# Performance work log

Hardware: AMD Instinct MI355X
Metric: run time of the kernel (lower is better)

## Reference

```python
import jax, jax.numpy as jnp
import numpy as np

EMBED_DIM = 1024
NUM_TOKENS = 32
TOKEN_DIM = 32  # ceil(1024/32)
CODEBOOK_SIZE = 256
BATCH = 32768
BETA = 0.25


def setup_inputs() -> dict:
    key = jax.random.key(0)
    ks = jax.random.split(key, 6)
    lim_e = 1.0 / np.sqrt(EMBED_DIM)
    lim_d = 1.0 / np.sqrt(NUM_TOKENS * TOKEN_DIM)
    lim_c = 1.0 / CODEBOOK_SIZE
    return {
        "skills": jax.random.normal(ks[0], (BATCH, EMBED_DIM), jnp.float32),
        "enc_w": jax.random.uniform(ks[1], (NUM_TOKENS * TOKEN_DIM, EMBED_DIM), jnp.float32, -lim_e, lim_e),
        "enc_b": jax.random.uniform(ks[2], (NUM_TOKENS * TOKEN_DIM,), jnp.float32, -lim_e, lim_e),
        "codebook": jax.random.uniform(ks[3], (CODEBOOK_SIZE, TOKEN_DIM), jnp.float32, -lim_c, lim_c),
        "dec_w": jax.random.uniform(ks[4], (EMBED_DIM, NUM_TOKENS * TOKEN_DIM), jnp.float32, -lim_d, lim_d),
        "dec_b": jax.random.uniform(ks[5], (EMBED_DIM,), jnp.float32, -lim_d, lim_d),
    }


def reference(skills, enc_w, enc_b, codebook, dec_w, dec_b):
    B = skills.shape[0]
    # encoder linear -> [B, num_tokens, token_dim]
    projected = (skills @ enc_w.T + enc_b).reshape(B, NUM_TOKENS, TOKEN_DIM)
    flat = projected.reshape(-1, TOKEN_DIM)  # [B*T, d]
    # squared-euclidean distances to codebook entries: [B*T, K]
    dists = (
        jnp.sum(flat * flat, axis=1, keepdims=True)
        - 2.0 * flat @ codebook.T
        + jnp.sum(codebook * codebook, axis=1)[None, :]
    )
    codes = jnp.argmin(dists, axis=1)  # [B*T]
    quantized = codebook[codes].reshape(B, NUM_TOKENS, TOKEN_DIM)
    # straight-through estimator
    st = projected + jax.lax.stop_gradient(quantized - projected)
    commitment = jnp.mean((projected - jax.lax.stop_gradient(quantized)) ** 2)
    codebook_loss = jnp.mean((quantized - jax.lax.stop_gradient(projected)) ** 2)
    vq_loss = codebook_loss + BETA * commitment
    reconstructed = st.reshape(B, NUM_TOKENS * TOKEN_DIM) @ dec_w.T + dec_b
    recon_loss = jnp.mean((reconstructed - skills) ** 2)
    loss = vq_loss + recon_loss
    return reconstructed, codes.reshape(B, NUM_TOKENS), loss
```

## Files before the change

### kernel.cpp

```cpp
#include <hip/hip_runtime.h>
#include <hip/hip_bf16.h>
#include <float.h>

#define NROWS 32768
#define EMB 1024
#define CBN 256
#define TD 32

#define OUT_CODES_OFF (33554432UL)
#define OUT_LOSS_OFF  (34603008UL)
#define TAU 1e-5f
#define INV_N (1.0f/33554432.0f)

typedef __attribute__((ext_vector_type(8))) short s16x8;
typedef __attribute__((ext_vector_type(4))) float f32x4;

__device__ __forceinline__ unsigned short bf16r(float x) {
    unsigned int u = __float_as_uint(x);
    unsigned int r = (u + 0x7FFFu + ((u >> 16) & 1u)) >> 16;
    return (unsigned short)r;
}
__device__ __forceinline__ float bf16f(unsigned short h) {
    return __uint_as_float(((unsigned int)h) << 16);
}
__device__ __forceinline__ void split8r(float4 v0, float4 v1, s16x8& h, s16x8& l) {
    float xs[8] = {v0.x, v0.y, v0.z, v0.w, v1.x, v1.y, v1.z, v1.w};
    #pragma unroll
    for (int e = 0; e < 8; ++e) {
        unsigned int u = __float_as_uint(xs[e]);
        unsigned short hh = (unsigned short)(u >> 16);
        h[e] = (short)hh;
        l[e] = (short)bf16r(xs[e] - bf16f(hh));
    }
}

__launch_bounds__(512, 1)
__global__ void k_enc(const float* __restrict__ skills,
                      const float* __restrict__ enc_w,
                      const float* __restrict__ enc_b,
                      const float* __restrict__ cb_g,
                      float* __restrict__ out)
{
    __shared__ __align__(16) char smem[125952];
    typedef unsigned short (*pu40)[40];
    pu40 Ah = (pu40)(smem);
    pu40 Al = (pu40)(smem + 10240);
    pu40 Bh = (pu40)(smem + 20480);
    pu40 Bl = (pu40)(smem + 30720);
    pu40 Sh = (pu40)(smem);
    pu40 Sl = (pu40)(smem + 40960);
    pu40 Ch = (pu40)(smem + 81920);
    pu40 Cl = (pu40)(smem + 102400);
    float* cnb = (float*)(smem + 122880);
    float* Fv  = (float*)(smem + 123904);

    const int tid = threadIdx.x;
    const int r0 = blockIdx.x * 128;
    const int wid = tid >> 6, lane = tid & 63;
    const int wm = wid >> 1, wn = wid & 1;
    const int mbase = wm * 32, nbase = wn * 64;
    const int lhi = lane >> 4, llo = lane & 15;
    const int srow = tid >> 2, sq = tid & 3;

    if (tid < 256) {
        const float4* cr = (const float4*)&cb_g[tid * 32];
        float s = 0.f;
        #pragma unroll
        for (int i = 0; i < 8; ++i) {
            float4 v = cr[i];
            float c[4] = {v.x, v.y, v.z, v.w};
            #pragma unroll
            for (int e = 0; e < 4; ++e) {
                unsigned int u = __float_as_uint(c[e]);
                unsigned short hh = (unsigned short)(u >> 16);
                Ch[tid][i*4+e] = hh;
                Cl[tid][i*4+e] = bf16r(c[e] - bf16f(hh));
                s = fmaf(c[e], c[e], s);
            }
        }
        cnb[tid] = s;
    }
    __syncthreads();

    float vq_local = 0.f;
    f32x4 acc[2][4];
    float4 ra0, ra1, rb0, rb1;

    {
        const float* ap = &skills[(size_t)(r0 + srow) * 1024 + sq * 8];
        ra0 = *(const float4*)ap; ra1 = *(const float4*)(ap + 4);
        const float* bp = &enc_w[(size_t)srow * 1024 + sq * 8];
        rb0 = *(const float4*)bp; rb1 = *(const float4*)(bp + 4);
    }

    for (int it = 0; it < 256; ++it) {
        const int nt = it >> 5, kt = it & 31;
        const int n0 = nt * 128;
        if (kt == 0) {
            #pragma unroll
            for (int mf = 0; mf < 2; ++mf)
                #pragma unroll
                for (int nf = 0; nf < 4; ++nf) acc[mf][nf] = (f32x4)0.f;
        }
        __syncthreads();
        {
            s16x8 h, l;
            split8r(ra0, ra1, h, l);
            *(s16x8*)&Ah[srow][sq * 8] = h;
            *(s16x8*)&Al[srow][sq * 8] = l;
            split8r(rb0, rb1, h, l);
            *(s16x8*)&Bh[srow][sq * 8] = h;
            *(s16x8*)&Bl[srow][sq * 8] = l;
        }
        __syncthreads();
        if (it < 255) {
            const int it2 = it + 1, nt2 = it2 >> 5, kt2 = it2 & 31;
            const float* ap = &skills[(size_t)(r0 + srow) * 1024 + kt2 * 32 + sq * 8];
            ra0 = *(const float4*)ap; ra1 = *(const float4*)(ap + 4);
            const float* bp = &enc_w[(size_t)(nt2 * 128 + srow) * 1024 + kt2 * 32 + sq * 8];
            rb0 = *(const float4*)bp; rb1 = *(const float4*)(bp + 4);
        }
        {
            s16x8 ah[2], al[2], bh[4], bl[4];
            #pragma unroll
            for (int mf = 0; mf < 2; ++mf) {
                const int row = mbase + mf * 16 + llo;
                ah[mf] = *(s16x8*)&Ah[row][lhi * 8];
                al[mf] = *(s16x8*)&Al[row][lhi * 8];
            }
            #pragma unroll
            for (int nf = 0; nf < 4; ++nf) {
                const int row = nbase + nf * 16 + llo;
                bh[nf] = *(s16x8*)&Bh[row][lhi * 8];
                bl[nf] = *(s16x8*)&Bl[row][lhi * 8];
            }
            #pragma unroll
            for (int mf = 0; mf < 2; ++mf)
                #pragma unroll
                for (int nf = 0; nf < 4; ++nf) {
                    acc[mf][nf] = __builtin_amdgcn_mfma_f32_16x16x32_bf16(ah[mf], bh[nf], acc[mf][nf], 0, 0, 0);
                    acc[mf][nf] = __builtin_amdgcn_mfma_f32_16x16x32_bf16(ah[mf], bl[nf], acc[mf][nf], 0, 0, 0);
                    acc[mf][nf] = __builtin_amdgcn_mfma_f32_16x16x32_bf16(al[mf], bh[nf], acc[mf][nf], 0, 0, 0);
                }
        }

        if (kt == 31) {
            __syncthreads();
            float fp[2][4][2];
            #pragma unroll
            for (int mf = 0; mf < 2; ++mf)
                #pragma unroll
                for (int r = 0; r < 4; ++r) { fp[mf][r][0] = 0.f; fp[mf][r][1] = 0.f; }

            #pragma unroll
            for (int mf = 0; mf < 2; ++mf)
                #pragma unroll
                for (int nf = 0; nf < 4; ++nf) {
                    const int n_local = nbase + nf * 16 + llo;
                    const float bias = enc_b[n0 + n_local];
                    const int tl = wn * 2 + (nf >> 1);
                    const int d = ((nf & 1) << 4) + llo;
                    #pragma unroll
                    for (int r = 0; r < 4; ++r) {
                        const int m_local = mbase + mf * 16 + lhi * 4 + r;
                        float val = acc[mf][nf][r] + bias;
                        unsigned int u = __float_as_uint(val);
                        unsigned short hh = (unsigned short)(u >> 16);
                        Sh[m_local * 4 + tl][d] = hh;
                        Sl[m_local * 4 + tl][d] = bf16r(val - bf16f(hh));
                        fp[mf][r][nf >> 1] = fmaf(val, val, fp[mf][r][nf >> 1]);
                    }
                }
            #pragma unroll
            for (int mf = 0; mf < 2; ++mf)
                #pragma unroll
                for (int r = 0; r < 4; ++r)
                    #pragma unroll
                    for (int tt = 0; tt < 2; ++tt) {
                        float f = fp[mf][r][tt];
                        f += __shfl_xor(f, 1); f += __shfl_xor(f, 2);
                        f += __shfl_xor(f, 4); f += __shfl_xor(f, 8);
                        if (llo == 0)
                            Fv[(mbase + mf * 16 + lhi * 4 + r) * 4 + wn * 2 + tt] = f;
                    }
            __syncthreads();

            #pragma unroll
            for (int gi = 0; gi < 4; ++gi) {
                const int g = wid * 4 + gi;
                const int tokrow = g * 16 + llo;
                s16x8 fh = *(s16x8*)&Sh[tokrow][lhi * 8];
                s16x8 fl = *(s16x8*)&Sl[tokrow][lhi * 8];
                float s1[4], s2[4]; int bj[4];
                #pragma unroll
                for (int r = 0; r < 4; ++r) { s1[r] = FLT_MAX; s2[r] = FLT_MAX; bj[r] = 0; }
                for (int jb = 0; jb < 16; ++jb) {
                    const int j = jb * 16 + llo;
                    s16x8 ch = *(s16x8*)&Ch[j][lhi * 8];
                    s16x8 cl = *(s16x8*)&Cl[j][lhi * 8];
                    f32x4 sc = (f32x4)0.f;
                    sc = __builtin_amdgcn_mfma_f32_16x16x32_bf16(fh, ch, sc, 0, 0, 0);
                    sc = __builtin_amdgcn_mfma_f32_16x16x32_bf16(fh, cl, sc, 0, 0, 0);
                    sc = __builtin_amdgcn_mfma_f32_16x16x32_bf16(fl, ch, sc, 0, 0, 0);
                    const float cnv = cnb[j];
                    #pragma unroll
                    for (int r = 0; r < 4; ++r) {
                        float s = fmaf(-2.f, sc[r], cnv);
                        if (s < s1[r])      { s2[r] = s1[r]; s1[r] = s; bj[r] = j; }
                        else if (s < s2[r]) { s2[r] = s; }
                    }
                }
                #pragma unroll
                for (int r = 0; r < 4; ++r) {
                    float a1 = s1[r], a2 = s2[r]; int aj = bj[r];
                    #pragma unroll
                    for (int off = 1; off <= 8; off <<= 1) {
                        float o1 = __shfl_xor(a1, off);
                        float o2 = __shfl_xor(a2, off);
                        int   oj = __shfl_xor(aj, off);
                        if (o1 < a1) { a2 = fminf(a1, o2); a1 = o1; aj = oj; }
                        else         { a2 = fminf(o1, a2); }
                    }
                    if (llo == 0) {
                        const int tok_local = g * 16 + lhi * 4 + r;
                        const float F = Fv[tok_local];
                        float cv = (a2 - a1 < TAU) ? (float)(aj + 512) : (float)aj;
                        const size_t tok = (size_t)(r0 + (tok_local >> 2)) * 32 + nt * 4 + (tok_local & 3);
                        out[OUT_CODES_OFF + tok] = cv;
                        vq_local += F + a1;
                    }
                }
            }
        }
    }
    {
        float v = vq_local;
        #pragma unroll
        for (int off = 32; off >= 1; off >>= 1) v += __shfl_xor(v, off);
        if (lane == 0) atomicAdd(&out[OUT_LOSS_OFF], v * (1.25f * INV_N));
    }
}

__launch_bounds__(256)
__global__ void k_fix(const float* __restrict__ skills,
                      const float* __restrict__ enc_w,
                      const float* __restrict__ enc_b,
                      const float* __restrict__ cb_g,
                      float* __restrict__ codes)
{
    __shared__ unsigned int cnt;
    __shared__ unsigned short list[256];

    const int tid = threadIdx.x;
    const int base = blockIdx.x * 256;

    if (tid == 0) cnt = 0;
    __syncthreads();
    {
        const int c = (int)codes[base + tid];
        if (c >= 512) {
            unsigned int ix = atomicAdd(&cnt, 1u);
            list[ix] = (unsigned short)tid;
        }
    }
    __syncthreads();
    const unsigned int n = cnt;
    if (n == 0) return;

    const int wv = tid >> 6, lane = tid & 63;
    const int d = lane & 31;

    for (unsigned int i = wv; i < n; i += 4) {
        const int tok = base + (int)list[i];
        const int row = tok >> 5;
        const int t   = tok & 31;

        const float4* s4 = (const float4*)&skills[(size_t)row * 1024];
        const float4* w4 = (const float4*)&enc_w[(size_t)(t * 32 + d) * 1024];
        float v1 = 0.f, v2 = 0.f, v3 = 0.f;
        for (int q = 0; q < 96; ++q) {
            float4 a = s4[q], b = w4[q];
            v1 = fmaf(a.x, b.x, v1); v1 = fmaf(a.y, b.y, v1);
            v1 = fmaf(a.z, b.z, v1); v1 = fmaf(a.w, b.w, v1);
        }
        for (int q = 96; q < 192; ++q) {
            float4 a = s4[q], b = w4[q];
            v2 = fmaf(a.x, b.x, v2); v2 = fmaf(a.y, b.y, v2);
            v2 = fmaf(a.z, b.z, v2); v2 = fmaf(a.w, b.w, v2);
        }
        for (int q = 192; q < 256; ++q) {
            float4 a = s4[q], b = w4[q];
            v3 = fmaf(a.x, b.x, v3); v3 = fmaf(a.y, b.y, v3);
            v3 = fmaf(a.z, b.z, v3); v3 = fmaf(a.w, b.w, v3);
        }
        const float pd = ((v1 + v2) + v3) + enc_b[t * 32 + d];

        float pv[32];
        #pragma unroll
        for (int dd = 0; dd < 32; ++dd) pv[dd] = __shfl(pd, dd);

        float F;
        {
            float s[32];
            #pragma unroll
            for (int dd = 0; dd < 32; ++dd) s[dd] = pv[dd] * pv[dd];
            float r[8];
            #pragma unroll
            for (int j = 0; j < 8; ++j) r[j] = ((s[j] + s[8+j]) + s[16+j]) + s[24+j];
            F = ((r[0] + r[1]) + (r[2] + r[3])) + ((r[4] + r[5]) + (r[6] + r[7]));
        }

        float bs = FLT_MAX; int bj = 0;
        for (int m = 0; m < 4; ++m) {
            const int j = m * 64 + lane;
            const float* cj = &cb_g[j * 32];
            float g = 0.f;
            #pragma unroll
            for (int dd = 0; dd < 32; ++dd) g = fmaf(pv[dd], cj[dd], g);
            float cs[32];
            #pragma unroll
            for (int dd = 0; dd < 32; ++dd) cs[dd] = cj[dd] * cj[dd];
            float r[8];
            #pragma unroll
            for (int jj = 0; jj < 8; ++jj) r[jj] = ((cs[jj] + cs[8+jj]) + cs[16+jj]) + cs[24+jj];
            float cn = ((r[0] + r[1]) + (r[2] + r[3])) + ((r[4] + r[5]) + (r[6] + r[7]));
            float dist = (F - 2.0f * g) + cn;
            if (dist < bs) { bs = dist; bj = j; }
        }
        #pragma unroll
        for (int off = 32; off >= 1; off >>= 1) {
            float os = __shfl_xor(bs, off);
            int   oj = __shfl_xor(bj, off);
            if (os < bs || (os == bs && oj < bj)) { bs = os; bj = oj; }
        }
        if (lane == 0) codes[tok] = (float)bj;
    }
}

__launch_bounds__(512)
__global__ void k_dec(const float* __restrict__ skills,
                      const float* __restrict__ cb_g,
                      const float* __restrict__ dec_w,
                      const float* __restrict__ dec_b,
                      const float* __restrict__ codes,
                      float* __restrict__ recon,
                      float* __restrict__ loss_out)
{
    __shared__ unsigned short Qt[128][40], Wt[128][40];

    const int tid = threadIdx.x;
    const int r0 = (blockIdx.x >> 3) * 128;
    const int n0 = (blockIdx.x & 7) * 128;
    const int wid = tid >> 6, lane = tid & 63;
    const int wm = wid >> 1, wn = wid & 1;
    const int mbase = wm * 32, nbase = wn * 64;
    const int lhi = lane >> 4, llo = lane & 15;
    const int srow = tid >> 2, sq = tid & 3;

    f32x4 acc[2][4];
    #pragma unroll
    for (int mf = 0; mf < 2; ++mf)
        #pragma unroll
        for (int nf = 0; nf < 4; ++nf) acc[mf][nf] = (f32x4)0.f;

    float4 q0, q1, w0, w1;
    int cnext;
    {
        const int c0 = ((int)codes[(size_t)(r0 + srow) * 32 + 0]) & 255;
        const float* cp = &cb_g[c0 * 32 + sq * 8];
        q0 = *(const float4*)cp; q1 = *(const float4*)(cp + 4);
        const float* wp = &dec_w[(size_t)(n0 + srow) * 1024 + sq * 8];
        w0 = *(const float4*)wp; w1 = *(const float4*)(wp + 4);
        cnext = ((int)codes[(size_t)(r0 + srow) * 32 + 1]) & 255;
    }

    for (int t = 0; t < 32; ++t) {
        __syncthreads();
        {
            float xs[8] = {q0.x, q0.y, q0.z, q0.w, q1.x, q1.y, q1.z, q1.w};
            s16x8 h;
            #pragma unroll
            for (int e = 0; e < 8; ++e) h[e] = (short)bf16r(xs[e]);
            *(s16x8*)&Qt[srow][sq * 8] = h;
            float ys[8] = {w0.x, w0.y, w0.z, w0.w, w1.x, w1.y, w1.z, w1.w};
            #pragma unroll
            for (int e = 0; e < 8; ++e) h[e] = (short)bf16r(ys[e]);
            *(s16x8*)&Wt[srow][sq * 8] = h;
        }
        __syncthreads();
        if (t < 31) {
            const float* cp = &cb_g[cnext * 32 + sq * 8];
            q0 = *(const float4*)cp; q1 = *(const float4*)(cp + 4);
            const float* wp = &dec_w[(size_t)(n0 + srow) * 1024 + (t + 1) * 32 + sq * 8];
            w0 = *(const float4*)wp; w1 = *(const float4*)(wp + 4);
            if (t < 30) cnext = ((int)codes[(size_t)(r0 + srow) * 32 + t + 2]) & 255;
        }
        s16x8 aq[2], bw[4];
        #pragma unroll
        for (int mf = 0; mf < 2; ++mf)
            aq[mf] = *(s16x8*)&Qt[mbase + mf * 16 + llo][lhi * 8];
        #pragma unroll
        for (int nf = 0; nf < 4; ++nf)
            bw[nf] = *(s16x8*)&Wt[nbase + nf * 16 + llo][lhi * 8];
        #pragma unroll
        for (int mf = 0; mf < 2; ++mf)
            #pragma unroll
            for (int nf = 0; nf < 4; ++nf)
                acc[mf][nf] = __builtin_amdgcn_mfma_f32_16x16x32_bf16(aq[mf], bw[nf], acc[mf][nf], 0, 0, 0);
    }

    float lsum = 0.f;
    #pragma unroll
    for (int mf = 0; mf < 2; ++mf)
        #pragma unroll
        for (int nf = 0; nf < 4; ++nf) {
            const int col = n0 + nbase + nf * 16 + llo;
            const float bias = dec_b[col];
            #pragma unroll
            for (int r = 0; r < 4; ++r) {
                const int row = r0 + mbase + mf * 16 + lhi * 4 + r;
                float rv = acc[mf][nf][r] + bias;
                float dv = rv - skills[(size_t)row * 1024 + col];
                lsum = fmaf(dv, dv, lsum);
                recon[(size_t)row * 1024 + col] = rv;
            }
        }
    #pragma unroll
    for (int off = 32; off >= 1; off >>= 1) lsum += __shfl_xor(lsum, off);
    if (lane == 0) atomicAdd(loss_out, lsum * INV_N);
}

extern "C" void kernel_launch(void* const* d_in, const int* in_sizes, int n_in,
                              void* d_out, int out_size, void* d_ws, size_t ws_size,
                              hipStream_t stream)
{
    const float* skills = (const float*)d_in[0];
    const float* enc_w  = (const float*)d_in[1];
    const float* enc_b  = (const float*)d_in[2];
    const float* cbg    = (const float*)d_in[3];
    const float* dec_w  = (const float*)d_in[4];
    const float* dec_b  = (const float*)d_in[5];
    float* out = (float*)d_out;

    hipMemsetAsync(out + OUT_LOSS_OFF, 0, 4, stream);
    k_enc<<<dim3(256), dim3(512), 0, stream>>>(skills, enc_w, enc_b, cbg, out);
    k_fix<<<dim3(4096), dim3(256), 0, stream>>>(skills, enc_w, enc_b, cbg, out + OUT_CODES_OFF);
    k_dec<<<dim3(2048), dim3(512), 0, stream>>>(skills, cbg, dec_w, dec_b,
                                                out + OUT_CODES_OFF, out, out + OUT_LOSS_OFF);
}
```

Before: 925.3 us.

## Pre-split skills and encoder weights into bf16 hi/lo arrays before GEMM

Adds a k_prep kernel that converts fp32 skills and enc_w into separate bf16 high and low arrays once. Previously the encoder GEMM redid this split for every tile load, so each skills tile was converted once per output column tile. The encoder now loads the bf16 pairs straight into shared memory with no conversion arithmetic in the main loop. The cost is an extra pass that reads and writes about 256 MB. The skills split is stored in the output buffer that k_enc also writes, which could be an aliasing hazard.

Measured after the change: 947.1 us. 2.4% more time.

```diff
diff --git a/kernel.cpp b/kernel.cpp
--- a/kernel.cpp
+++ b/kernel.cpp
@@ -34,9 +34,27 @@
     }
 }
 
+__global__ void k_prep(const float* __restrict__ in,
+                       unsigned short* __restrict__ hi,
+                       unsigned short* __restrict__ lo,
+                       int n8)
+{
+    const int i = blockIdx.x * 256 + threadIdx.x;
+    if (i >= n8) return;
+    const float4* p = (const float4*)(in + (size_t)i * 8);
+    s16x8 h, l;
+    split8r(p[0], p[1], h, l);
+    *(s16x8*)(hi + (size_t)i * 8) = h;
+    *(s16x8*)(lo + (size_t)i * 8) = l;
+}
+
+template <bool PREW>
 __launch_bounds__(512, 1)
-__global__ void k_enc(const float* __restrict__ skills,
+__global__ void k_enc(const unsigned short* __restrict__ s_hi,
+                      const unsigned short* __restrict__ s_lo,
                       const float* __restrict__ enc_w,
+                      const unsigned short* __restrict__ w_hi,
+                      const unsigned short* __restrict__ w_lo,
                       const float* __restrict__ enc_b,
                       const float* __restrict__ cb_g,
                       float* __restrict__ out)
@@ -84,13 +102,20 @@
 
     float vq_local = 0.f;
     f32x4 acc[2][4];
-    float4 ra0, ra1, rb0, rb1;
+    s16x8 rah, ral, rbh, rbl;
 
     {
-        const float* ap = &skills[(size_t)(r0 + srow) * 1024 + sq * 8];
-        ra0 = *(const float4*)ap; ra1 = *(const float4*)(ap + 4);
-        const float* bp = &enc_w[(size_t)srow * 1024 + sq * 8];
-        rb0 = *(const float4*)bp; rb1 = *(const float4*)(bp + 4);
+        const size_t aoff = (size_t)(r0 + srow) * 1024 + sq * 8;
+        rah = *(const s16x8*)(s_hi + aoff);
+        ral = *(const s16x8*)(s_lo + aoff);
+        if (PREW) {
+            const size_t boff = (size_t)srow * 1024 + sq * 8;
+            rbh = *(const s16x8*)(w_hi + boff);
+            rbl = *(const s16x8*)(w_lo + boff);
+        } else {
+            const float* bp = &enc_w[(size_t)srow * 1024 + sq * 8];
+            split8r(*(const float4*)bp, *(const float4*)(bp + 4), rbh, rbl);
+        }
     }
 
     for (int it = 0; it < 256; ++it) {
@@ -103,22 +128,24 @@
                 for (int nf = 0; nf < 4; ++nf) acc[mf][nf] = (f32x4)0.f;
         }
         __syncthreads();
-        {
-            s16x8 h, l;
-            split8r(ra0, ra1, h, l);
-            *(s16x8*)&Ah[srow][sq * 8] = h;
-            *(s16x8*)&Al[srow][sq * 8] = l;
-            split8r(rb0, rb1, h, l);
-            *(s16x8*)&Bh[srow][sq * 8] = h;
-            *(s16x8*)&Bl[srow][sq * 8] = l;
-        }
+        *(s16x8*)&Ah[srow][sq * 8] = rah;
+        *(s16x8*)&Al[srow][sq * 8] = ral;
+        *(s16x8*)&Bh[srow][sq * 8] = rbh;
+        *(s16x8*)&Bl[srow][sq * 8] = rbl;
         __syncthreads();
         if (it < 255) {
             const int it2 = it + 1, nt2 = it2 >> 5, kt2 = it2 & 31;
-            const float* ap = &skills[(size_t)(r0 + srow) * 1024 + kt2 * 32 + sq * 8];
-            ra0 = *(const float4*)ap; ra1 = *(const float4*)(ap + 4);
-            const float* bp = &enc_w[(size_t)(nt2 * 128 + srow) * 1024 + kt2 * 32 + sq * 8];
-            rb0 = *(const float4*)bp; rb1 = *(const float4*)(bp + 4);
+            const size_t aoff = (size_t)(r0 + srow) * 1024 + kt2 * 32 + sq * 8;
+            rah = *(const s16x8*)(s_hi + aoff);
+            ral = *(const s16x8*)(s_lo + aoff);
+            if (PREW) {
+                const size_t boff = (size_t)(nt2 * 128 + srow) * 1024 + kt2 * 32 + sq * 8;
+                rbh = *(const s16x8*)(w_hi + boff);
+                rbl = *(const s16x8*)(w_lo + boff);
+            } else {
+                const float* bp = &enc_w[(size_t)(nt2 * 128 + srow) * 1024 + kt2 * 32 + sq * 8];
+                split8r(*(const float4*)bp, *(const float4*)(bp + 4), rbh, rbl);
+            }
         }
         {
             s16x8 ah[2], al[2], bh[4], bl[4];
@@ -442,8 +469,23 @@
     const float* dec_b  = (const float*)d_in[5];
     float* out = (float*)d_out;
 
+    unsigned short* s_hi = (unsigned short*)out;
+    unsigned short* s_lo = s_hi + 33554432UL;
+
     hipMemsetAsync(out + OUT_LOSS_OFF, 0, 4, stream);
-    k_enc<<<dim3(256), dim3(512), 0, stream>>>(skills, enc_w, enc_b, cbg, out);
+    k_prep<<<dim3(16384), dim3(256), 0, stream>>>(skills, s_hi, s_lo, 4194304);
+
+    const bool prew = (ws_size >= (4UL * 1048576UL + 64UL));
+    unsigned short* w_hi = (unsigned short*)d_ws;
+    unsigned short* w_lo = w_hi + 1048576UL;
+    if (prew) {
+        k_prep<<<dim3(512), dim3(256), 0, stream>>>(enc_w, w_hi, w_lo, 131072);
+        k_enc<true><<<dim3(256), dim3(512), 0, stream>>>(s_hi, s_lo, enc_w, w_hi, w_lo,
+                                                         enc_b, cbg, out);
+    } else {
+        k_enc<false><<<dim3(256), dim3(512), 0, stream>>>(s_hi, s_lo, enc_w, w_hi, w_lo,
+                                                          enc_b, cbg, out);
+    }
     k_fix<<<dim3(4096), dim3(256), 0, stream>>>(skills, enc_w, enc_b, cbg, out + OUT_CODES_OFF);
     k_dec<<<dim3(2048), dim3(512), 0, stream>>>(skills, cbg, dec_w, dec_b,
                                                 out + OUT_CODES_OFF, out, out + OUT_LOSS_OFF);
```
